# Optimization experiments

Measured on AMD Instinct MI355X. Metric: run time of the kernel, lower is better.

Reference implementation:

```python
import jax, jax.numpy as jnp
import numpy as np

# TT configuration (matches init_kwargs)
P = (100, 100, 100)      # tt_p_shapes, prod = num_embeddings = 1e6
Q = (4, 4, 8)            # tt_q_shapes, prod = embedding_dim = 128
R = (1, 32, 32, 1)       # tt_ranks padded with boundary 1s
D = 128                  # embedding_dim
B = 4096                 # batch size (number of bags)
H = 50                   # pooling factor (history length)
NNZ = B * H              # total indices


def setup_inputs() -> dict:
    key = jax.random.key(0)
    k1, k2, k3, k4 = jax.random.split(key, 4)
    # TT cores, stored flattened along trailing dims like TT-Rec:
    # core_i : [p_i, r_i * q_i * r_{i+1}]
    sigma = 0.1
    core0 = sigma * jax.random.normal(k1, (P[0], R[0] * Q[0] * R[1]), dtype=jnp.float32)
    core1 = sigma * jax.random.normal(k2, (P[1], R[1] * Q[1] * R[2]), dtype=jnp.float32)
    core2 = sigma * jax.random.normal(k3, (P[2], R[2] * Q[2] * R[3]), dtype=jnp.float32)
    indices = jax.random.randint(k4, (NNZ,), 0, P[0] * P[1] * P[2], dtype=jnp.int32)
    lengths = jnp.full((B,), H, dtype=jnp.int32)
    return {"indices": indices, "lengths": lengths,
            "core0": core0, "core1": core1, "core2": core2}


def reference(indices, lengths, core0, core1, core2):
    n = indices.shape[0]
    # mixed-radix decomposition of flat row index over p-shapes
    i1 = indices // (P[1] * P[2])
    i2 = (indices // P[2]) % P[1]
    i3 = indices % P[2]
    # gather per-index TT core slices
    a = core0[i1].reshape(n, Q[0], R[1])          # [n, q1, r1]
    b = core1[i2].reshape(n, R[1], Q[1], R[2])    # [n, r1, q2, r2]
    c = core2[i3].reshape(n, R[2], Q[2])          # [n, r2, q3]
    # TT contraction chain reconstructing each embedding row
    ab = jnp.einsum('nar,nrbs->nabs', a, b).reshape(n, Q[0] * Q[1], R[2])  # [n, q1*q2, r2]
    emb = jnp.einsum('nms,nsc->nmc', ab, c).reshape(n, D)                  # [n, D]
    # bag sum-pooling: rowidx = repeat_interleave(arange(B), lengths)
    batch = lengths.shape[0]
    rowidx = jnp.repeat(jnp.arange(batch, dtype=jnp.int32), lengths,
                        total_repeat_length=n)
    out = jax.ops.segment_sum(emb, rowidx, num_segments=batch)             # [B, D]
    return out
```

## Files before the change

### kernel.cpp

```cpp
#include <hip/hip_runtime.h>
#include <hip/hip_bf16.h>


#define P0 100
#define P1 100
#define P2 100
#define Q0 4
#define Q1 4
#define Q2 8
#define DIM 128
#define NPAIR (P0 * P1)

typedef __attribute__((ext_vector_type(8))) short short8v;
typedef __attribute__((ext_vector_type(4))) float f32x4;

__global__ __launch_bounds__(128) void prep(const int* __restrict__ lengths, int B,
                                            const float* __restrict__ core0,
                                            const float* __restrict__ core1,
                                            const float* __restrict__ core2,
                                            int* __restrict__ offsets,
                                            __hip_bfloat16* __restrict__ bfrag,
                                            __hip_bfloat16* __restrict__ ab) {
    int bid = blockIdx.x;
    int t = threadIdx.x;
    if (bid == 0) {
        __shared__ int part[128];
        int per = (B + 127) / 128;
        int s = 0;
        for (int k = 0; k < per; ++k) {
            int i = t * per + k;
            s += (i < B) ? lengths[i] : 0;
        }
        part[t] = s;
        __syncthreads();
        for (int d = 1; d < 128; d <<= 1) {
            int v = (t >= d) ? part[t - d] : 0;
            __syncthreads();
            part[t] += v;
            __syncthreads();
        }
        int run = part[t] - s;
        for (int k = 0; k < per; ++k) {
            int i = t * per + k;
            if (i < B) { offsets[i] = run; run += lengths[i]; }
        }
        if (t == 127) offsets[B] = part[127];
    } else if (bid <= P2) {
        if (t < 64 && !(t & 8)) {
            int i3 = bid - 1;
            int h = t >> 4, c3 = t & 7;
            const float* crow = core2 + (size_t)i3 * (32 * Q2);
            __hip_bfloat16* o = bfrag + (size_t)i3 * 256 + h * 64 + c3 * 8;
#pragma unroll
            for (int j = 0; j < 8; ++j)
                o[j] = __float2bfloat16(crow[(h * 8 + j) * Q2 + c3]);
        }
    } else {
        int p12 = bid - 1 - P2;
        int i1 = p12 / P1;
        int i2 = p12 - i1 * P1;
        __shared__ float a_lds[128];
        a_lds[t] = core0[i1 * 128 + t];
        __syncthreads();
        const float* brow = core1 + (size_t)i2 * 4096;
        float acc0 = 0.f, acc1 = 0.f, acc2 = 0.f, acc3 = 0.f;
#pragma unroll
        for (int r = 0; r < 32; ++r) {
            float bv = brow[r * 128 + t];
            acc0 += a_lds[r] * bv;
            acc1 += a_lds[32 + r] * bv;
            acc2 += a_lds[64 + r] * bv;
            acc3 += a_lds[96 + r] * bv;
        }
        __hip_bfloat16* o = ab + (size_t)p12 * 512;
        o[t]       = __float2bfloat16(acc0);
        o[128 + t] = __float2bfloat16(acc1);
        o[256 + t] = __float2bfloat16(acc2);
        o[384 + t] = __float2bfloat16(acc3);
    }
}

__global__ __launch_bounds__(256) void bag_pool(const int* __restrict__ indices, int n,
                                                const int* __restrict__ offsets, int B,
                                                const char* __restrict__ ab,
                                                const char* __restrict__ bfrag,
                                                float* __restrict__ out) {
    int wave = threadIdx.x >> 6;
    int lane = threadIdx.x & 63;
    int bag = blockIdx.x * 4 + wave;
    if (bag >= B) return;

    int start = offsets[bag];
    int end = offsets[bag + 1];
    if (bag == B - 1 && end < n) end = n;
    if (end > n) end = n;
    if (start > n) start = n;
    int cnt = end - start;

    int aoff = (lane & 15) * 64 + (lane >> 4) * 16;
    int boff = (lane >> 4) * 128 + (lane & 7) * 16;

    f32x4 acc0 = {0.f, 0.f, 0.f, 0.f};
    f32x4 acc1 = {0.f, 0.f, 0.f, 0.f};
    f32x4 acc2 = {0.f, 0.f, 0.f, 0.f};
    f32x4 acc3 = {0.f, 0.f, 0.f, 0.f};

    for (int base = 0; base < cnt; base += 64) {
        int m = cnt - base;
        if (m > 64) m = 64;
        unsigned idx = 0;
        if (lane < m) idx = (unsigned)indices[start + base + lane];
        unsigned p = idx / 100u;
        unsigned i3 = idx - p * 100u;
        int abo = (int)(p << 10);
        int bfo = (int)(i3 << 9);

        int j = 0;
        for (; j + 3 < m; j += 4) {
            int A0 = __shfl(abo, j),     B0 = __shfl(bfo, j);
            int A1 = __shfl(abo, j + 1), B1 = __shfl(bfo, j + 1);
            int A2 = __shfl(abo, j + 2), B2 = __shfl(bfo, j + 2);
            int A3 = __shfl(abo, j + 3), B3 = __shfl(bfo, j + 3);
            short8v a0 = *(const short8v*)(ab + A0 + aoff);
            short8v b0 = *(const short8v*)(bfrag + B0 + boff);
            short8v a1 = *(const short8v*)(ab + A1 + aoff);
            short8v b1 = *(const short8v*)(bfrag + B1 + boff);
            short8v a2 = *(const short8v*)(ab + A2 + aoff);
            short8v b2 = *(const short8v*)(bfrag + B2 + boff);
            short8v a3 = *(const short8v*)(ab + A3 + aoff);
            short8v b3 = *(const short8v*)(bfrag + B3 + boff);
            acc0 = __builtin_amdgcn_mfma_f32_16x16x32_bf16(a0, b0, acc0, 0, 0, 0);
            acc1 = __builtin_amdgcn_mfma_f32_16x16x32_bf16(a1, b1, acc1, 0, 0, 0);
            acc2 = __builtin_amdgcn_mfma_f32_16x16x32_bf16(a2, b2, acc2, 0, 0, 0);
            acc3 = __builtin_amdgcn_mfma_f32_16x16x32_bf16(a3, b3, acc3, 0, 0, 0);
        }
        for (; j < m; ++j) {
            int A0 = __shfl(abo, j), B0 = __shfl(bfo, j);
            short8v a0 = *(const short8v*)(ab + A0 + aoff);
            short8v b0 = *(const short8v*)(bfrag + B0 + boff);
            acc0 = __builtin_amdgcn_mfma_f32_16x16x32_bf16(a0, b0, acc0, 0, 0, 0);
        }
    }
    f32x4 acc = (acc0 + acc1) + (acc2 + acc3);

    int col = lane & 15;
    if (col < 8) {
        int rb = (lane >> 4) * 4;
        float* orow = out + (size_t)bag * DIM;
#pragma unroll
        for (int q = 0; q < 4; ++q)
            orow[(rb + q) * 8 + col] = acc[q];
    }
}

__global__ __launch_bounds__(128) void fallback_pool(const int* __restrict__ indices,
                                                     int n, int B,
                                                     const float* __restrict__ core0,
                                                     const float* __restrict__ core1,
                                                     const float* __restrict__ core2,
                                                     float* __restrict__ out) {
    int bag = blockIdx.x;
    int d = threadIdx.x;
    int m = d >> 3, c3 = d & 7;
    int a_ = m >> 2, b_ = m & 3;
    int H = n / B;
    float acc = 0.f;
    for (int j = bag * H; j < (bag + 1) * H; ++j) {
        int idx = indices[j];
        int i1 = idx / (P1 * P2);
        int rem = idx - i1 * (P1 * P2);
        int i2 = rem / P2;
        int i3 = rem - i2 * P2;
        const float* a = core0 + (size_t)i1 * 128;
        const float* b = core1 + (size_t)i2 * 4096;
        const float* c = core2 + (size_t)i3 * 256;
        float e = 0.f;
        for (int s = 0; s < 32; ++s) {
            float abv = 0.f;
            for (int r = 0; r < 32; ++r)
                abv += a[a_ * 32 + r] * b[r * 128 + b_ * 32 + s];
            e += abv * c[s * 8 + c3];
        }
        acc += e;
    }
    out[(size_t)bag * DIM + d] = acc;
}

extern "C" void kernel_launch(void* const* d_in, const int* in_sizes, int n_in,
                              void* d_out, int out_size, void* d_ws, size_t ws_size,
                              hipStream_t stream) {
    const int* indices = (const int*)d_in[0];
    const int* lengths = (const int*)d_in[1];
    const float* core0 = (const float*)d_in[2];
    const float* core1 = (const float*)d_in[3];
    const float* core2 = (const float*)d_in[4];
    float* out = (float*)d_out;
    int n = in_sizes[0];
    int B = in_sizes[1];

    const size_t OFF_OFFSETS = 0;
    const size_t OFF_BFRAG = 32768;
    const size_t OFF_AB = 131072;
    const size_t REQ = OFF_AB + (size_t)NPAIR * 1024;

    if (ws_size >= REQ) {
        int* offsets = (int*)((char*)d_ws + OFF_OFFSETS);
        __hip_bfloat16* bfrag = (__hip_bfloat16*)((char*)d_ws + OFF_BFRAG);
        __hip_bfloat16* abt = (__hip_bfloat16*)((char*)d_ws + OFF_AB);

        prep<<<1 + P2 + NPAIR, 128, 0, stream>>>(lengths, B, core0, core1, core2,
                                                 offsets, bfrag, abt);
        bag_pool<<<(B + 3) / 4, 256, 0, stream>>>(indices, n, offsets, B,
                                                  (const char*)abt, (const char*)bfrag, out);
    } else {
        fallback_pool<<<B, 128, 0, stream>>>(indices, n, B, core0, core1, core2, out);
    }
}
```

Before: 43.65 us.

## Reuse core1 slice across ten core0 rows in prep and split bags across waves

The prep kernel now launches 1000 blocks of 256 threads instead of 10000 blocks. Each block keeps one core1 slice in registers and computes the AB products for ten core0 rows, so core1 is re-read far less often and there are fewer tiny blocks. The scan block moves to the end of the grid. In bag_pool, each bag is split across two waves whose partial sums are combined through LDS, and the gather loop is double-buffered: loads for the next group of four indices are issued before the current MFMAs, with readlane in place of shfl. This adds register pressure and a block-wide barrier, and the AB kernel reads core0 through scalar/global loads that may not be coalesced.

```diff
diff --git a/kernel.cpp b/kernel.cpp
--- a/kernel.cpp
+++ b/kernel.cpp
@@ -5,16 +5,15 @@
 #define P0 100
 #define P1 100
 #define P2 100
-#define Q0 4
-#define Q1 4
 #define Q2 8
 #define DIM 128
 #define NPAIR (P0 * P1)
+#define NAB_BLOCKS 1000
 
 typedef __attribute__((ext_vector_type(8))) short short8v;
 typedef __attribute__((ext_vector_type(4))) float f32x4;
 
-__global__ __launch_bounds__(128) void prep(const int* __restrict__ lengths, int B,
+__global__ __launch_bounds__(256) void prep(const int* __restrict__ lengths, int B,
                                             const float* __restrict__ core0,
                                             const float* __restrict__ core1,
                                             const float* __restrict__ core2,
@@ -23,9 +22,41 @@
                                             __hip_bfloat16* __restrict__ ab) {
     int bid = blockIdx.x;
     int t = threadIdx.x;
-    if (bid == 0) {
-        __shared__ int part[128];
-        int per = (B + 127) / 128;
+    if (bid < NAB_BLOCKS) {
+        int i2 = bid % P1;
+        int g10 = bid / P1;
+        int col = t & 127;
+        int h = t >> 7;
+        const float* brow = core1 + (size_t)i2 * 4096;
+        float v[32];
+#pragma unroll
+        for (int r = 0; r < 32; ++r) v[r] = brow[r * 128 + col];
+        for (int q = 0; q < 10; ++q) {
+            int i1 = g10 * 10 + q;
+            const float* arow = core0 + (size_t)i1 * 128;
+            float acc0 = 0.f, acc1 = 0.f;
+#pragma unroll
+            for (int r = 0; r < 32; ++r) {
+                acc0 = fmaf(arow[(2 * h) * 32 + r], v[r], acc0);
+                acc1 = fmaf(arow[(2 * h + 1) * 32 + r], v[r], acc1);
+            }
+            __hip_bfloat16* o = ab + (size_t)(i1 * P1 + i2) * 512;
+            o[(2 * h) * 128 + col]     = __float2bfloat16(acc0);
+            o[(2 * h + 1) * 128 + col] = __float2bfloat16(acc1);
+        }
+    } else if (bid < NAB_BLOCKS + P2) {
+        if (t < 64 && !(t & 8)) {
+            int i3 = bid - NAB_BLOCKS;
+            int h = t >> 4, c3 = t & 7;
+            const float* crow = core2 + (size_t)i3 * (32 * Q2);
+            __hip_bfloat16* o = bfrag + (size_t)i3 * 256 + h * 64 + c3 * 8;
+#pragma unroll
+            for (int j = 0; j < 8; ++j)
+                o[j] = __float2bfloat16(crow[(h * 8 + j) * Q2 + c3]);
+        }
+    } else {
+        __shared__ int part[256];
+        int per = (B + 255) / 256;
         int s = 0;
         for (int k = 0; k < per; ++k) {
             int i = t * per + k;
@@ -33,10 +64,10 @@
         }
         part[t] = s;
         __syncthreads();
-        for (int d = 1; d < 128; d <<= 1) {
-            int v = (t >= d) ? part[t - d] : 0;
+        for (int d = 1; d < 256; d <<= 1) {
+            int vv = (t >= d) ? part[t - d] : 0;
             __syncthreads();
-            part[t] += v;
+            part[t] += vv;
             __syncthreads();
         }
         int run = part[t] - s;
@@ -44,40 +75,37 @@
             int i = t * per + k;
             if (i < B) { offsets[i] = run; run += lengths[i]; }
         }
-        if (t == 127) offsets[B] = part[127];
-    } else if (bid <= P2) {
-        if (t < 64 && !(t & 8)) {
-            int i3 = bid - 1;
-            int h = t >> 4, c3 = t & 7;
-            const float* crow = core2 + (size_t)i3 * (32 * Q2);
-            __hip_bfloat16* o = bfrag + (size_t)i3 * 256 + h * 64 + c3 * 8;
-#pragma unroll
-            for (int j = 0; j < 8; ++j)
-                o[j] = __float2bfloat16(crow[(h * 8 + j) * Q2 + c3]);
-        }
-    } else {
-        int p12 = bid - 1 - P2;
-        int i1 = p12 / P1;
-        int i2 = p12 - i1 * P1;
-        __shared__ float a_lds[128];
-        a_lds[t] = core0[i1 * 128 + t];
-        __syncthreads();
-        const float* brow = core1 + (size_t)i2 * 4096;
-        float acc0 = 0.f, acc1 = 0.f, acc2 = 0.f, acc3 = 0.f;
-#pragma unroll
-        for (int r = 0; r < 32; ++r) {
-            float bv = brow[r * 128 + t];
-            acc0 += a_lds[r] * bv;
-            acc1 += a_lds[32 + r] * bv;
-            acc2 += a_lds[64 + r] * bv;
-            acc3 += a_lds[96 + r] * bv;
-        }
-        __hip_bfloat16* o = ab + (size_t)p12 * 512;
-        o[t]       = __float2bfloat16(acc0);
-        o[128 + t] = __float2bfloat16(acc1);
-        o[256 + t] = __float2bfloat16(acc2);
-        o[384 + t] = __float2bfloat16(acc3);
-    }
+        if (t == 255) offsets[B] = part[255];
+    }
+}
+
+
+#define FETCH(g, fa, fb) {                                          \
+    int _j = (g) << 2;                                              \
+    int _A0 = __builtin_amdgcn_readlane(abo, _j);                   \
+    int _B0 = __builtin_amdgcn_readlane(bfo, _j);                   \
+    int _A1 = __builtin_amdgcn_readlane(abo, _j + 1);               \
+    int _B1 = __builtin_amdgcn_readlane(bfo, _j + 1);               \
+    int _A2 = __builtin_amdgcn_readlane(abo, _j + 2);               \
+    int _B2 = __builtin_amdgcn_readlane(bfo, _j + 2);               \
+    int _A3 = __builtin_amdgcn_readlane(abo, _j + 3);               \
+    int _B3 = __builtin_amdgcn_readlane(bfo, _j + 3);               \
+    fa##0 = *(const short8v*)(ab + _A0 + aoff);                     \
+    fb##0 = *(const short8v*)(bfrag + _B0 + boff);                  \
+    fa##1 = *(const short8v*)(ab + _A1 + aoff);                     \
+    fb##1 = *(const short8v*)(bfrag + _B1 + boff);                  \
+    fa##2 = *(const short8v*)(ab + _A2 + aoff);                     \
+    fb##2 = *(const short8v*)(bfrag + _B2 + boff);                  \
+    fa##3 = *(const short8v*)(ab + _A3 + aoff);                     \
+    fb##3 = *(const short8v*)(bfrag + _B3 + boff);                  \
+}
+
+#define MFMAG(fa, fb, g) {                                                        \
+    int _rem = m - ((g) << 2);                                                    \
+    acc0 = __builtin_amdgcn_mfma_f32_16x16x32_bf16(fa##0, fb##0, acc0, 0, 0, 0);  \
+    if (_rem > 1) acc1 = __builtin_amdgcn_mfma_f32_16x16x32_bf16(fa##1, fb##1, acc1, 0, 0, 0); \
+    if (_rem > 2) acc2 = __builtin_amdgcn_mfma_f32_16x16x32_bf16(fa##2, fb##2, acc2, 0, 0, 0); \
+    if (_rem > 3) acc3 = __builtin_amdgcn_mfma_f32_16x16x32_bf16(fa##3, fb##3, acc3, 0, 0, 0); \
 }
 
 __global__ __launch_bounds__(256) void bag_pool(const int* __restrict__ indices, int n,
@@ -85,17 +113,24 @@
                                                 const char* __restrict__ ab,
                                                 const char* __restrict__ bfrag,
                                                 float* __restrict__ out) {
-    int wave = threadIdx.x >> 6;
+    int w = threadIdx.x >> 6;
     int lane = threadIdx.x & 63;
-    int bag = blockIdx.x * 4 + wave;
-    if (bag >= B) return;
-
-    int start = offsets[bag];
-    int end = offsets[bag + 1];
-    if (bag == B - 1 && end < n) end = n;
-    if (end > n) end = n;
-    if (start > n) start = n;
+    int bag = blockIdx.x * 2 + (w >> 1);
+    int half = w & 1;
+
+    int start = 0, end = 0;
+    if (bag < B) {
+        start = offsets[bag];
+        end = offsets[bag + 1];
+        if (bag == B - 1 && end < n) end = n;
+        if (end > n) end = n;
+        if (start > n) start = n;
+        if (end < start) end = start;
+    }
     int cnt = end - start;
+    int c0 = (cnt + 1) >> 1;
+    int mystart = start + (half ? c0 : 0);
+    int mycnt = half ? (cnt - c0) : c0;
 
     int aoff = (lane & 15) * 64 + (lane >> 4) * 16;
     int boff = (lane >> 4) * 128 + (lane & 7) * 16;
@@ -105,51 +140,45 @@
     f32x4 acc2 = {0.f, 0.f, 0.f, 0.f};
     f32x4 acc3 = {0.f, 0.f, 0.f, 0.f};
 
-    for (int base = 0; base < cnt; base += 64) {
-        int m = cnt - base;
+    for (int cb = 0; cb < mycnt; cb += 64) {
+        int m = mycnt - cb;
         if (m > 64) m = 64;
         unsigned idx = 0;
-        if (lane < m) idx = (unsigned)indices[start + base + lane];
+        if (lane < m) idx = (unsigned)indices[mystart + cb + lane];
         unsigned p = idx / 100u;
         unsigned i3 = idx - p * 100u;
         int abo = (int)(p << 10);
         int bfo = (int)(i3 << 9);
 
-        int j = 0;
-        for (; j + 3 < m; j += 4) {
-            int A0 = __shfl(abo, j),     B0 = __shfl(bfo, j);
-            int A1 = __shfl(abo, j + 1), B1 = __shfl(bfo, j + 1);
-            int A2 = __shfl(abo, j + 2), B2 = __shfl(bfo, j + 2);
-            int A3 = __shfl(abo, j + 3), B3 = __shfl(bfo, j + 3);
-            short8v a0 = *(const short8v*)(ab + A0 + aoff);
-            short8v b0 = *(const short8v*)(bfrag + B0 + boff);
-            short8v a1 = *(const short8v*)(ab + A1 + aoff);
-            short8v b1 = *(const short8v*)(bfrag + B1 + boff);
-            short8v a2 = *(const short8v*)(ab + A2 + aoff);
-            short8v b2 = *(const short8v*)(bfrag + B2 + boff);
-            short8v a3 = *(const short8v*)(ab + A3 + aoff);
-            short8v b3 = *(const short8v*)(bfrag + B3 + boff);
-            acc0 = __builtin_amdgcn_mfma_f32_16x16x32_bf16(a0, b0, acc0, 0, 0, 0);
-            acc1 = __builtin_amdgcn_mfma_f32_16x16x32_bf16(a1, b1, acc1, 0, 0, 0);
-            acc2 = __builtin_amdgcn_mfma_f32_16x16x32_bf16(a2, b2, acc2, 0, 0, 0);
-            acc3 = __builtin_amdgcn_mfma_f32_16x16x32_bf16(a3, b3, acc3, 0, 0, 0);
-        }
-        for (; j < m; ++j) {
-            int A0 = __shfl(abo, j), B0 = __shfl(bfo, j);
-            short8v a0 = *(const short8v*)(ab + A0 + aoff);
-            short8v b0 = *(const short8v*)(bfrag + B0 + boff);
-            acc0 = __builtin_amdgcn_mfma_f32_16x16x32_bf16(a0, b0, acc0, 0, 0, 0);
+        int G = (m + 3) >> 2;
+        short8v fa0, fa1, fa2, fa3, fb0, fb1, fb2, fb3;
+        short8v ga0, ga1, ga2, ga3, gb0, gb1, gb2, gb3;
+        FETCH(0, fa, fb);
+        int g = 0;
+        while (true) {
+            if (g + 1 < G) FETCH(g + 1, ga, gb);
+            MFMAG(fa, fb, g);
+            ++g; if (g >= G) break;
+            if (g + 1 < G) FETCH(g + 1, fa, fb);
+            MFMAG(ga, gb, g);
+            ++g; if (g >= G) break;
         }
     }
     f32x4 acc = (acc0 + acc1) + (acc2 + acc3);
 
-    int col = lane & 15;
-    if (col < 8) {
-        int rb = (lane >> 4) * 4;
-        float* orow = out + (size_t)bag * DIM;
-#pragma unroll
-        for (int q = 0; q < 4; ++q)
-            orow[(rb + q) * 8 + col] = acc[q];
+    __shared__ f32x4 red[2][64];
+    if (half) red[w >> 1][lane] = acc;
+    __syncthreads();
+    if (!half) {
+        acc += red[w >> 1][lane];
+        int col = lane & 15;
+        if (bag < B && col < 8) {
+            int rb = (lane >> 4) * 4;
+            float* orow = out + (size_t)bag * DIM;
+#pragma unroll
+            for (int q = 0; q < 4; ++q)
+                orow[(rb + q) * 8 + col] = acc[q];
+        }
     }
 }
 
@@ -205,13 +234,13 @@
 
     if (ws_size >= REQ) {
         int* offsets = (int*)((char*)d_ws + OFF_OFFSETS);
-        __hip_bfloat16* bfrag = (__hip_bfloat16*)((char*)d_ws + OFF_BFRAG);
+        __hip_bfloat16* bfragp = (__hip_bfloat16*)((char*)d_ws + OFF_BFRAG);
         __hip_bfloat16* abt = (__hip_bfloat16*)((char*)d_ws + OFF_AB);
 
-        prep<<<1 + P2 + NPAIR, 128, 0, stream>>>(lengths, B, core0, core1, core2,
-                                                 offsets, bfrag, abt);
-        bag_pool<<<(B + 3) / 4, 256, 0, stream>>>(indices, n, offsets, B,
-                                                  (const char*)abt, (const char*)bfrag, out);
+        prep<<<NAB_BLOCKS + P2 + 1, 256, 0, stream>>>(lengths, B, core0, core1, core2,
+                                                      offsets, bfragp, abt);
+        bag_pool<<<(B + 1) / 2, 256, 0, stream>>>(indices, n, offsets, B,
+                                                  (const char*)abt, (const char*)bfragp, out);
     } else {
         fallback_pool<<<B, 128, 0, stream>>>(indices, n, B, core0, core1, core2, out);
     }
```

Result: slower. 56.62 us (+29.7%).

## Split each bag across two waves and reduce partial sums through LDS

Applied to the files above, without the earlier changes.

Each bag's index range is now split in half and handled by two waves, so one block covers 2 bags instead of 4 and the grid doubles. The halves' MFMA accumulators are combined through shared memory after a block barrier before the row is written. This aims to double the number of waves in flight and shorten each wave's serial chain of gathers and MFMAs. In exchange it adds an LDS round-trip and a __syncthreads, and launch bounds now request 6 blocks per CU, which limits registers.

```diff
diff --git a/kernel.cpp b/kernel.cpp
--- a/kernel.cpp
+++ b/kernel.cpp
@@ -80,22 +80,29 @@
     }
 }
 
-__global__ __launch_bounds__(256) void bag_pool(const int* __restrict__ indices, int n,
-                                                const int* __restrict__ offsets, int B,
-                                                const char* __restrict__ ab,
-                                                const char* __restrict__ bfrag,
-                                                float* __restrict__ out) {
-    int wave = threadIdx.x >> 6;
+__global__ __launch_bounds__(256, 6) void bag_pool(const int* __restrict__ indices, int n,
+                                                   const int* __restrict__ offsets, int B,
+                                                   const char* __restrict__ ab,
+                                                   const char* __restrict__ bfrag,
+                                                   float* __restrict__ out) {
+    int w = threadIdx.x >> 6;
     int lane = threadIdx.x & 63;
-    int bag = blockIdx.x * 4 + wave;
-    if (bag >= B) return;
-
-    int start = offsets[bag];
-    int end = offsets[bag + 1];
-    if (bag == B - 1 && end < n) end = n;
-    if (end > n) end = n;
-    if (start > n) start = n;
+    int bag = blockIdx.x * 2 + (w >> 1);
+    int half = w & 1;
+
+    int start = 0, end = 0;
+    if (bag < B) {
+        start = offsets[bag];
+        end = offsets[bag + 1];
+        if (bag == B - 1 && end < n) end = n;
+        if (end > n) end = n;
+        if (start > n) start = n;
+        if (end < start) end = start;
+    }
     int cnt = end - start;
+    int c0 = (cnt + 1) >> 1;
+    int mystart = start + (half ? c0 : 0);
+    int mycnt = half ? (cnt - c0) : c0;
 
     int aoff = (lane & 15) * 64 + (lane >> 4) * 16;
     int boff = (lane >> 4) * 128 + (lane & 7) * 16;
@@ -105,11 +112,11 @@
     f32x4 acc2 = {0.f, 0.f, 0.f, 0.f};
     f32x4 acc3 = {0.f, 0.f, 0.f, 0.f};
 
-    for (int base = 0; base < cnt; base += 64) {
-        int m = cnt - base;
+    for (int cb = 0; cb < mycnt; cb += 64) {
+        int m = mycnt - cb;
         if (m > 64) m = 64;
         unsigned idx = 0;
-        if (lane < m) idx = (unsigned)indices[start + base + lane];
+        if (lane < m) idx = (unsigned)indices[mystart + cb + lane];
         unsigned p = idx / 100u;
         unsigned i3 = idx - p * 100u;
         int abo = (int)(p << 10);
@@ -143,13 +150,19 @@
     }
     f32x4 acc = (acc0 + acc1) + (acc2 + acc3);
 
-    int col = lane & 15;
-    if (col < 8) {
-        int rb = (lane >> 4) * 4;
-        float* orow = out + (size_t)bag * DIM;
+    __shared__ f32x4 red[2][64];
+    if (half) red[w >> 1][lane] = acc;
+    __syncthreads();
+    if (!half) {
+        acc += red[w >> 1][lane];
+        int col = lane & 15;
+        if (bag < B && col < 8) {
+            int rb = (lane >> 4) * 4;
+            float* orow = out + (size_t)bag * DIM;
 #pragma unroll
-        for (int q = 0; q < 4; ++q)
-            orow[(rb + q) * 8 + col] = acc[q];
+            for (int q = 0; q < 4; ++q)
+                orow[(rb + q) * 8 + col] = acc[q];
+        }
     }
 }
 
@@ -205,13 +218,13 @@
 
     if (ws_size >= REQ) {
         int* offsets = (int*)((char*)d_ws + OFF_OFFSETS);
-        __hip_bfloat16* bfrag = (__hip_bfloat16*)((char*)d_ws + OFF_BFRAG);
+        __hip_bfloat16* bfragp = (__hip_bfloat16*)((char*)d_ws + OFF_BFRAG);
         __hip_bfloat16* abt = (__hip_bfloat16*)((char*)d_ws + OFF_AB);
 
         prep<<<1 + P2 + NPAIR, 128, 0, stream>>>(lengths, B, core0, core1, core2,
-                                                 offsets, bfrag, abt);
-        bag_pool<<<(B + 3) / 4, 256, 0, stream>>>(indices, n, offsets, B,
-                                                  (const char*)abt, (const char*)bfrag, out);
+                                                 offsets, bfragp, abt);
+        bag_pool<<<(B + 1) / 2, 256, 0, stream>>>(indices, n, offsets, B,
+                                                  (const char*)abt, (const char*)bfragp, out);
     } else {
         fallback_pool<<<B, 128, 0, stream>>>(indices, n, B, core0, core1, core2, out);
     }
```

New measurement: 44.17 us. No clear change (+1.2%).
